# Kernel tuning notes

Hardware: AMD Instinct MI355X
Metric: run time of the kernel (lower is better)

The kernel has to match this reference:

```python
import jax, jax.numpy as jnp
import numpy as np

B, Q, K, D = 32, 1024, 1024, 64
MASK_VAL = -1000000.0  # matches torch source's -1e6 fill


def setup_inputs() -> dict:
    key = jax.random.key(0)
    kq, kk, kv, kl = jax.random.split(key, 4)
    return {
        "queries": jax.random.normal(kq, (B, Q, D), dtype=jnp.float32),
        "keys": jax.random.normal(kk, (B, K, D), dtype=jnp.float32),
        "values": jax.random.normal(kv, (B, K, D), dtype=jnp.float32),
        "valid_lens": jax.random.randint(kl, (B,), 1, K + 1, dtype=jnp.int64),
    }


def reference(queries, keys, values, valid_lens):
    d = queries.shape[-1]
    # [B, Q, K] scores
    scores = jnp.einsum("bqd,bkd->bqk", queries, keys) / jnp.sqrt(jnp.asarray(d, queries.dtype))
    # 1D valid_lens -> same length mask for every query row of a batch element
    kv_pos = jnp.arange(scores.shape[-1])  # [K]
    mask = kv_pos[None, None, :] < valid_lens[:, None, None]  # [B, 1, K] broadcast
    scores = jnp.where(mask, scores, MASK_VAL)
    attn = jax.nn.softmax(scores, axis=-1)
    # dropout p=0.0 -> identity
    return jnp.einsum("bqk,bkd->bqd", attn, values)
```

## Files before the change

### kernel.cpp

```cpp
#include <hip/hip_runtime.h>
#include <hip/hip_bf16.h>

#define NB 32
#define NQ 1024
#define NK 1024
#define ND 64
#define BK 64
#define M_FIX 16.0f

typedef __attribute__((ext_vector_type(8))) __bf16 bf16x8;
typedef __attribute__((ext_vector_type(8))) short  s16x8;
typedef __attribute__((ext_vector_type(4))) float  f32x4;

static __device__ __forceinline__ short f2bf(float f) {
  unsigned u = __builtin_bit_cast(unsigned, f);
  u += 0x7fffu + ((u >> 16) & 1u);
  return (short)(u >> 16);
}

static __device__ __forceinline__ int swzoff(int row, int gcol) {
  return row * 64 + (((gcol ^ (row & 7)) & 7) << 3);
}

#define GLD_LDS16(gp, lp)                                              \
  __builtin_amdgcn_global_load_lds(                                    \
      (const __attribute__((address_space(1))) void*)(gp),             \
      (__attribute__((address_space(3))) void*)(lp), 16, 0, 0)

__launch_bounds__(256)
__global__ void prep_kv(const float* __restrict__ Kp, const float* __restrict__ Vp,
                        const int* __restrict__ VLp,
                        short* __restrict__ Kb, short* __restrict__ Vt) {
  __shared__ __align__(16) short T[64 * 72];
  const int wg = blockIdx.x;
  const int b  = wg >> 4;
  const int kt = wg & 15;

  const bool is64 = (VLp[1] == 0);
  const int  len  = is64 ? VLp[2 * b] : VLp[b];
  if (kt * 64 >= len) return;

  const int tid = threadIdx.x;

  {
    const int key = tid >> 2, d0 = (tid & 3) * 16, g0 = (tid & 3) * 2;
    const float* src = Kp + ((size_t)(b * NK + kt * 64 + key)) * ND + d0;
    short out[16];
#pragma unroll
    for (int i = 0; i < 16; i += 4) {
      float4 v = *(const float4*)(src + i);
      out[i] = f2bf(v.x); out[i + 1] = f2bf(v.y);
      out[i + 2] = f2bf(v.z); out[i + 3] = f2bf(v.w);
    }
    short* dtile = Kb + ((size_t)(b * 16 + kt)) * 4096;
    *(s16x8*)&dtile[swzoff(key, g0)]     = *(const s16x8*)out;
    *(s16x8*)&dtile[swzoff(key, g0 + 1)] = *(const s16x8*)(out + 8);
  }

  {
    const int vkey = tid & 63, vd0 = (tid >> 6) * 16;
    const float* src = Vp + ((size_t)(b * NK + kt * 64 + vkey)) * ND + vd0;
#pragma unroll
    for (int i = 0; i < 4; ++i) {
      float4 v = *(const float4*)(src + i * 4);
      T[(vd0 + i * 4 + 0) * 72 + vkey] = f2bf(v.x);
      T[(vd0 + i * 4 + 1) * 72 + vkey] = f2bf(v.y);
      T[(vd0 + i * 4 + 2) * 72 + vkey] = f2bf(v.z);
      T[(vd0 + i * 4 + 3) * 72 + vkey] = f2bf(v.w);
    }
  }
  __syncthreads();
  {
    const int d = tid >> 2, c = (tid & 3) * 16, g0 = (tid & 3) * 2;
    short* vtile = Vt + ((size_t)(b * 16 + kt)) * 4096;
    *(s16x8*)&vtile[swzoff(d, g0)]     = *(const s16x8*)&T[d * 72 + c];
    *(s16x8*)&vtile[swzoff(d, g0 + 1)] = *(const s16x8*)&T[d * 72 + c + 8];
  }
}

__launch_bounds__(512, 4)
__global__ void attn_fwd(const float* __restrict__ Qp,
                         const short* __restrict__ Kb,
                         const short* __restrict__ Vt,
                         const int* __restrict__ VLp,
                         float* __restrict__ Op) {
  __shared__ __align__(16) short SM[40960];
  char* smb = (char*)SM;

  const int wg  = blockIdx.x;
  const int swz = (wg & 7) * 64 + (wg >> 3);
  const int b   = swz >> 4;
  const int qb  = swz & 15;

  const int tid  = threadIdx.x;
  const int wid  = tid >> 6;
  const int lane = tid & 63;
  const int l16  = lane & 15;
  const int grp  = lane >> 4;
  const int esw  = l16 & 7;
  const int qgrp = wid >> 1;
  const int par  = wid & 1;

  const bool is64 = (VLp[1] == 0);
  const int  len  = is64 ? VLp[2 * b] : VLp[b];
  const int  ntiles = (len + BK - 1) >> 6;
  const int  nsup   = (ntiles + 1) >> 1;
  const int  remLast = len - ((ntiles - 1) << 6);

  const float qscale = 0.125f * 1.44269504088896341f;

  bf16x8 qf[2];
  {
    const float* qsrc = Qp + ((size_t)(b * NQ + qb * 64 + qgrp * 16 + l16)) * ND + grp * 8;
#pragma unroll
    for (int k2 = 0; k2 < 2; ++k2) {
      float4 a = *(const float4*)(qsrc + k2 * 32);
      float4 c = *(const float4*)(qsrc + k2 * 32 + 4);
      s16x8 t;
      t[0] = f2bf(a.x * qscale); t[1] = f2bf(a.y * qscale);
      t[2] = f2bf(a.z * qscale); t[3] = f2bf(a.w * qscale);
      t[4] = f2bf(c.x * qscale); t[5] = f2bf(c.y * qscale);
      t[6] = f2bf(c.z * qscale); t[7] = f2bf(c.w * qscale);
      qf[k2] = __builtin_bit_cast(bf16x8, t);
    }
  }

  int ka0 = par * 8192 + l16 * 128 + ((((0 * 4 + grp) ^ esw)) << 4);
  int ka1 = par * 8192 + l16 * 128 + ((((1 * 4 + grp) ^ esw)) << 4);
  int pra[2], pwa[8];
#pragma unroll
  for (int ks = 0; ks < 2; ++ks)
    pra[ks] = 65536 + wid * 2048 + l16 * 128 + (((ks * 4 + grp) ^ esw) << 4);
#pragma unroll
  for (int n = 0; n < 4; ++n)
#pragma unroll
    for (int a = 0; a < 2; ++a)
      pwa[n * 2 + a] = 65536 + wid * 2048 + l16 * 128
                     + ((((2 * n + (grp >> 1)) ^ esw)) << 4) + (((2 * grp + a) & 3) << 2);

  const char* kgp = (const char*)(Kb + (size_t)b * 16 * 4096) + tid * 16;
  const char* vgp = (const char*)(Vt + (size_t)b * 16 * 4096) + tid * 16;
  const int dstW = wid * 1024;

  const f32x4 minit = {-M_FIX, -M_FIX, -M_FIX, -M_FIX};
  const f32x4 vzero = {0.f, 0.f, 0.f, 0.f};
  f32x4 oacc[4];
#pragma unroll
  for (int i = 0; i < 4; ++i) oacc[i] = vzero;
  float lrun = 0.f;

  int bufB = 0;

  GLD_LDS16(kgp,        smb + dstW);
  GLD_LDS16(kgp + 8192, smb + 8192 + dstW);
  GLD_LDS16(vgp,        smb + 32768 + dstW);
  GLD_LDS16(vgp + 8192, smb + 40960 + dstW);
  kgp += 16384; vgp += 16384;

  for (int it = 0; it < nsup; ++it) {
    asm volatile("s_waitcnt vmcnt(0)" ::: "memory");
    __builtin_amdgcn_sched_barrier(0);
    __builtin_amdgcn_s_barrier();
    __builtin_amdgcn_sched_barrier(0);

    if (it + 1 < nsup) {
      const int nb = bufB ^ 16384;
      GLD_LDS16(kgp,        smb + nb + dstW);
      GLD_LDS16(kgp + 8192, smb + nb + 8192 + dstW);
      GLD_LDS16(vgp,        smb + 32768 + nb + dstW);
      GLD_LDS16(vgp + 8192, smb + 32768 + nb + 8192 + dstW);
      kgp += 16384; vgp += 16384;
    }

    const int myt = 2 * it + par;
    if (myt < ntiles) {
      f32x4 sc[4];
      __builtin_amdgcn_s_setprio(1);
#pragma unroll
      for (int n = 0; n < 4; ++n) {
        bf16x8 kf0 = __builtin_bit_cast(bf16x8,
            *(const s16x8*)(smb + bufB + ka0 + n * 2048));
        bf16x8 kf1 = __builtin_bit_cast(bf16x8,
            *(const s16x8*)(smb + bufB + ka1 + n * 2048));
        f32x4 acc = __builtin_amdgcn_mfma_f32_16x16x32_bf16(kf0, qf[0], minit, 0, 0, 0);
        acc = __builtin_amdgcn_mfma_f32_16x16x32_bf16(kf1, qf[1], acc, 0, 0, 0);
        sc[n] = acc;
      }
      __builtin_amdgcn_s_setprio(0);

      if (myt == ntiles - 1) {
#pragma unroll
        for (int n = 0; n < 4; ++n)
#pragma unroll
          for (int r = 0; r < 4; ++r) {
            float x = (n * 16 + grp * 4 + r < remLast) ? sc[n][r] : -128.0f;
            float pv = exp2f(x);
            sc[n][r] = pv;
            lrun += pv;
          }
      } else {
#pragma unroll
        for (int n = 0; n < 4; ++n)
#pragma unroll
          for (int r = 0; r < 4; ++r) {
            float pv = exp2f(sc[n][r]);
            sc[n][r] = pv;
            lrun += pv;
          }
      }

#pragma unroll
      for (int n = 0; n < 4; ++n)
#pragma unroll
        for (int a = 0; a < 2; ++a) {
          int d;
          asm("v_cvt_pk_bf16_f32 %0, %1, %2"
              : "=v"(d) : "v"(sc[n][2 * a]), "v"(sc[n][2 * a + 1]));
          *(int*)(smb + pwa[n * 2 + a]) = d;
        }

      asm volatile("s_waitcnt lgkmcnt(0)" ::: "memory");
      __builtin_amdgcn_sched_barrier(0);

      bf16x8 pf[2];
#pragma unroll
      for (int ks = 0; ks < 2; ++ks)
        pf[ks] = __builtin_bit_cast(bf16x8, *(const s16x8*)(smb + pra[ks]));

      __builtin_amdgcn_s_setprio(1);
#pragma unroll
      for (int nd = 0; nd < 4; ++nd) {
        bf16x8 vf0 = __builtin_bit_cast(bf16x8,
            *(const s16x8*)(smb + bufB + ka0 + 32768 + nd * 2048));
        bf16x8 vf1 = __builtin_bit_cast(bf16x8,
            *(const s16x8*)(smb + bufB + ka1 + 32768 + nd * 2048));
        oacc[nd] = __builtin_amdgcn_mfma_f32_16x16x32_bf16(pf[0], vf0, oacc[nd], 0, 0, 0);
        oacc[nd] = __builtin_amdgcn_mfma_f32_16x16x32_bf16(pf[1], vf1, oacc[nd], 0, 0, 0);
      }
      __builtin_amdgcn_s_setprio(0);
    }

    bufB ^= 16384;
  }

  __syncthreads();
  float* CB = (float*)SM;
  const int crow = qgrp * 64 + lane;
  if (par == 1) {
    float* dst = CB + (size_t)crow * 20;
#pragma unroll
    for (int nd = 0; nd < 4; ++nd) *(f32x4*)(dst + nd * 4) = oacc[nd];
    dst[16] = lrun;
  }
  __syncthreads();
  if (par == 0) {
    const float* src = CB + (size_t)crow * 20;
#pragma unroll
    for (int nd = 0; nd < 4; ++nd) oacc[nd] += *(const f32x4*)(src + nd * 4);
    float l = lrun + src[16];
    l += __shfl_xor(l, 16);
    l += __shfl_xor(l, 32);
    const float inv = 1.0f / l;
    float invr[4];
#pragma unroll
    for (int r = 0; r < 4; ++r)
      invr[r] = __shfl(inv, (lane & 48) | (grp * 4 + r));

    float* obase = Op + ((size_t)(b * NQ + qb * 64 + qgrp * 16)) * ND;
#pragma unroll
    for (int nd = 0; nd < 4; ++nd)
#pragma unroll
      for (int r = 0; r < 4; ++r)
        obase[(grp * 4 + r) * ND + nd * 16 + l16] = oacc[nd][r] * invr[r];
  }
}

extern "C" void kernel_launch(void* const* d_in, const int* in_sizes, int n_in,
                              void* d_out, int out_size, void* d_ws, size_t ws_size,
                              hipStream_t stream) {
  const float* Qp = (const float*)d_in[0];
  const float* Kp = (const float*)d_in[1];
  const float* Vp = (const float*)d_in[2];
  const int*   VL = (const int*)d_in[3];
  float* Op = (float*)d_out;

  short* Kb = (short*)d_ws;
  short* Vt = Kb + (size_t)NB * NK * ND;

  prep_kv<<<dim3(NB * 16), dim3(256), 0, stream>>>(Kp, Vp, VL, Kb, Vt);
  attn_fwd<<<dim3(NB * 16), dim3(512), 0, stream>>>(Qp, Kb, Vt, VL, Op);
}
```

Baseline: 28.99 us.

## Split attention into 32-query blocks with 32-key tiles and 4-way KV split

Each workgroup now handles 32 query rows instead of 64, and the grid doubles to 1024 blocks. Each of 4 warps per query group processes its own 32-key tile, with K/V re-laid out into 32-key tiles in the prep kernel. Shared memory is halved and single-buffered with a second barrier before refilling, so launch bounds can allow 8 blocks per CU. The aim is more parallelism and occupancy for variable valid lengths. The cost is losing the double-buffered prefetch overlap, an extra barrier per iteration, and a 4-way partial-sum reduction at the end.

```diff
diff --git a/kernel.cpp b/kernel.cpp
--- a/kernel.cpp
+++ b/kernel.cpp
@@ -5,7 +5,6 @@
 #define NQ 1024
 #define NK 1024
 #define ND 64
-#define BK 64
 #define M_FIX 16.0f
 
 typedef __attribute__((ext_vector_type(8))) __bf16 bf16x8;
@@ -16,10 +15,6 @@
   unsigned u = __builtin_bit_cast(unsigned, f);
   u += 0x7fffu + ((u >> 16) & 1u);
   return (short)(u >> 16);
-}
-
-static __device__ __forceinline__ int swzoff(int row, int gcol) {
-  return row * 64 + (((gcol ^ (row & 7)) & 7) << 3);
 }
 
 #define GLD_LDS16(gp, lp)                                              \
@@ -44,6 +39,7 @@
 
   {
     const int key = tid >> 2, d0 = (tid & 3) * 16, g0 = (tid & 3) * 2;
+    const int row = key & 31, st = key >> 5;
     const float* src = Kp + ((size_t)(b * NK + kt * 64 + key)) * ND + d0;
     short out[16];
 #pragma unroll
@@ -52,9 +48,9 @@
       out[i] = f2bf(v.x); out[i + 1] = f2bf(v.y);
       out[i + 2] = f2bf(v.z); out[i + 3] = f2bf(v.w);
     }
-    short* dtile = Kb + ((size_t)(b * 16 + kt)) * 4096;
-    *(s16x8*)&dtile[swzoff(key, g0)]     = *(const s16x8*)out;
-    *(s16x8*)&dtile[swzoff(key, g0 + 1)] = *(const s16x8*)(out + 8);
+    short* dtile = Kb + ((size_t)(b * 32 + kt * 2 + st)) * 2048;
+    *(s16x8*)&dtile[row * 64 + (((g0    ) ^ (row & 7)) << 3)] = *(const s16x8*)out;
+    *(s16x8*)&dtile[row * 64 + (((g0 + 1) ^ (row & 7)) << 3)] = *(const s16x8*)(out + 8);
   }
 
   {
@@ -71,47 +67,50 @@
   }
   __syncthreads();
   {
-    const int d = tid >> 2, c = (tid & 3) * 16, g0 = (tid & 3) * 2;
-    short* vtile = Vt + ((size_t)(b * 16 + kt)) * 4096;
-    *(s16x8*)&vtile[swzoff(d, g0)]     = *(const s16x8*)&T[d * 72 + c];
-    *(s16x8*)&vtile[swzoff(d, g0 + 1)] = *(const s16x8*)&T[d * 72 + c + 8];
-  }
-}
-
-__launch_bounds__(512, 4)
+    const int d = tid >> 2, q4 = tid & 3;
+    const int st = q4 >> 1, g0 = (q4 & 1) * 2;
+    short* vtile = Vt + ((size_t)(b * 32 + kt * 2 + st)) * 2048;
+    const short* s = &T[d * 72 + q4 * 16];
+    *(s16x8*)&vtile[d * 32 + ((((g0    ) ^ (d & 3)) & 3) << 3)] = *(const s16x8*)s;
+    *(s16x8*)&vtile[d * 32 + ((((g0 + 1) ^ (d & 3)) & 3) << 3)] = *(const s16x8*)(s + 8);
+  }
+}
+
+__launch_bounds__(512, 8)
 __global__ void attn_fwd(const float* __restrict__ Qp,
                          const short* __restrict__ Kb,
                          const short* __restrict__ Vt,
                          const int* __restrict__ VLp,
                          float* __restrict__ Op) {
-  __shared__ __align__(16) short SM[40960];
+  __shared__ __align__(16) short SM[20480];
   char* smb = (char*)SM;
 
   const int wg  = blockIdx.x;
-  const int swz = (wg & 7) * 64 + (wg >> 3);
-  const int b   = swz >> 4;
-  const int qb  = swz & 15;
+  const int swz = (wg & 7) * 128 + (wg >> 3);
+  const int b   = swz >> 5;
+  const int qb  = swz & 31;
 
   const int tid  = threadIdx.x;
   const int wid  = tid >> 6;
   const int lane = tid & 63;
   const int l16  = lane & 15;
   const int grp  = lane >> 4;
-  const int esw  = l16 & 7;
-  const int qgrp = wid >> 1;
-  const int par  = wid & 1;
+  const int e7   = l16 & 7;
+  const int e3   = l16 & 3;
+  const int qgrp = wid >> 2;
+  const int par  = wid & 3;
 
   const bool is64 = (VLp[1] == 0);
   const int  len  = is64 ? VLp[2 * b] : VLp[b];
-  const int  ntiles = (len + BK - 1) >> 6;
-  const int  nsup   = (ntiles + 1) >> 1;
-  const int  remLast = len - ((ntiles - 1) << 6);
+  const int  ntiles = (len + 31) >> 5;
+  const int  nsup   = (ntiles + 3) >> 2;
+  const int  remLast = len - ((ntiles - 1) << 5);
 
   const float qscale = 0.125f * 1.44269504088896341f;
 
   bf16x8 qf[2];
   {
-    const float* qsrc = Qp + ((size_t)(b * NQ + qb * 64 + qgrp * 16 + l16)) * ND + grp * 8;
+    const float* qsrc = Qp + ((size_t)(b * NQ + qb * 32 + qgrp * 16 + l16)) * ND + grp * 8;
 #pragma unroll
     for (int k2 = 0; k2 < 2; ++k2) {
       float4 a = *(const float4*)(qsrc + k2 * 32);
@@ -125,21 +124,15 @@
     }
   }
 
-  int ka0 = par * 8192 + l16 * 128 + ((((0 * 4 + grp) ^ esw)) << 4);
-  int ka1 = par * 8192 + l16 * 128 + ((((1 * 4 + grp) ^ esw)) << 4);
-  int pra[2], pwa[8];
-#pragma unroll
-  for (int ks = 0; ks < 2; ++ks)
-    pra[ks] = 65536 + wid * 2048 + l16 * 128 + (((ks * 4 + grp) ^ esw) << 4);
-#pragma unroll
-  for (int n = 0; n < 4; ++n)
-#pragma unroll
-    for (int a = 0; a < 2; ++a)
-      pwa[n * 2 + a] = 65536 + wid * 2048 + l16 * 128
-                     + ((((2 * n + (grp >> 1)) ^ esw)) << 4) + (((2 * grp + a) & 3) << 2);
-
-  const char* kgp = (const char*)(Kb + (size_t)b * 16 * 4096) + tid * 16;
-  const char* vgp = (const char*)(Vt + (size_t)b * 16 * 4096) + tid * 16;
+  const int ka  = par * 4096 + l16 * 128;
+  const int kb0 = ka + (((0 + grp) ^ e7) << 4);
+  const int kb1 = ka + (((4 + grp) ^ e7) << 4);
+  const int va  = 16384 + par * 4096 + l16 * 64 + (((grp ^ e3) & 3) << 4);
+  const int pb  = 32768 + wid * 1024 + l16 * 64;
+  const int pra = pb + (((grp ^ e3) & 3) << 4);
+
+  const char* kgp = (const char*)(Kb + (size_t)b * 32 * 2048) + tid * 16;
+  const char* vgp = (const char*)(Vt + (size_t)b * 32 * 2048) + tid * 16;
   const int dstW = wid * 1024;
 
   const f32x4 minit = {-M_FIX, -M_FIX, -M_FIX, -M_FIX};
@@ -149,12 +142,10 @@
   for (int i = 0; i < 4; ++i) oacc[i] = vzero;
   float lrun = 0.f;
 
-  int bufB = 0;
-
   GLD_LDS16(kgp,        smb + dstW);
   GLD_LDS16(kgp + 8192, smb + 8192 + dstW);
-  GLD_LDS16(vgp,        smb + 32768 + dstW);
-  GLD_LDS16(vgp + 8192, smb + 40960 + dstW);
+  GLD_LDS16(vgp,        smb + 16384 + dstW);
+  GLD_LDS16(vgp + 8192, smb + 24576 + dstW);
   kgp += 16384; vgp += 16384;
 
   for (int it = 0; it < nsup; ++it) {
@@ -163,25 +154,14 @@
     __builtin_amdgcn_s_barrier();
     __builtin_amdgcn_sched_barrier(0);
 
-    if (it + 1 < nsup) {
-      const int nb = bufB ^ 16384;
-      GLD_LDS16(kgp,        smb + nb + dstW);
-      GLD_LDS16(kgp + 8192, smb + nb + 8192 + dstW);
-      GLD_LDS16(vgp,        smb + 32768 + nb + dstW);
-      GLD_LDS16(vgp + 8192, smb + 32768 + nb + 8192 + dstW);
-      kgp += 16384; vgp += 16384;
-    }
-
-    const int myt = 2 * it + par;
+    const int myt = 4 * it + par;
     if (myt < ntiles) {
-      f32x4 sc[4];
+      f32x4 sc[2];
       __builtin_amdgcn_s_setprio(1);
 #pragma unroll
-      for (int n = 0; n < 4; ++n) {
-        bf16x8 kf0 = __builtin_bit_cast(bf16x8,
-            *(const s16x8*)(smb + bufB + ka0 + n * 2048));
-        bf16x8 kf1 = __builtin_bit_cast(bf16x8,
-            *(const s16x8*)(smb + bufB + ka1 + n * 2048));
+      for (int n = 0; n < 2; ++n) {
+        bf16x8 kf0 = __builtin_bit_cast(bf16x8, *(const s16x8*)(smb + kb0 + n * 2048));
+        bf16x8 kf1 = __builtin_bit_cast(bf16x8, *(const s16x8*)(smb + kb1 + n * 2048));
         f32x4 acc = __builtin_amdgcn_mfma_f32_16x16x32_bf16(kf0, qf[0], minit, 0, 0, 0);
         acc = __builtin_amdgcn_mfma_f32_16x16x32_bf16(kf1, qf[1], acc, 0, 0, 0);
         sc[n] = acc;
@@ -190,7 +170,7 @@
 
       if (myt == ntiles - 1) {
 #pragma unroll
-        for (int n = 0; n < 4; ++n)
+        for (int n = 0; n < 2; ++n)
 #pragma unroll
           for (int r = 0; r < 4; ++r) {
             float x = (n * 16 + grp * 4 + r < remLast) ? sc[n][r] : -128.0f;
@@ -200,7 +180,7 @@
           }
       } else {
 #pragma unroll
-        for (int n = 0; n < 4; ++n)
+        for (int n = 0; n < 2; ++n)
 #pragma unroll
           for (int r = 0; r < 4; ++r) {
             float pv = exp2f(sc[n][r]);
@@ -210,54 +190,62 @@
       }
 
 #pragma unroll
-      for (int n = 0; n < 4; ++n)
+      for (int n = 0; n < 2; ++n)
 #pragma unroll
         for (int a = 0; a < 2; ++a) {
           int d;
           asm("v_cvt_pk_bf16_f32 %0, %1, %2"
               : "=v"(d) : "v"(sc[n][2 * a]), "v"(sc[n][2 * a + 1]));
-          *(int*)(smb + pwa[n * 2 + a]) = d;
+          *(int*)(smb + pb + ((((2 * n + (grp >> 1)) ^ e3) & 3) << 4)
+                        + (((grp * 2 + a) & 3) << 2)) = d;
         }
 
       asm volatile("s_waitcnt lgkmcnt(0)" ::: "memory");
       __builtin_amdgcn_sched_barrier(0);
 
-      bf16x8 pf[2];
-#pragma unroll
-      for (int ks = 0; ks < 2; ++ks)
-        pf[ks] = __builtin_bit_cast(bf16x8, *(const s16x8*)(smb + pra[ks]));
+      bf16x8 pf = __builtin_bit_cast(bf16x8, *(const s16x8*)(smb + pra));
 
       __builtin_amdgcn_s_setprio(1);
 #pragma unroll
       for (int nd = 0; nd < 4; ++nd) {
-        bf16x8 vf0 = __builtin_bit_cast(bf16x8,
-            *(const s16x8*)(smb + bufB + ka0 + 32768 + nd * 2048));
-        bf16x8 vf1 = __builtin_bit_cast(bf16x8,
-            *(const s16x8*)(smb + bufB + ka1 + 32768 + nd * 2048));
-        oacc[nd] = __builtin_amdgcn_mfma_f32_16x16x32_bf16(pf[0], vf0, oacc[nd], 0, 0, 0);
-        oacc[nd] = __builtin_amdgcn_mfma_f32_16x16x32_bf16(pf[1], vf1, oacc[nd], 0, 0, 0);
+        bf16x8 vf = __builtin_bit_cast(bf16x8, *(const s16x8*)(smb + va + nd * 1024));
+        oacc[nd] = __builtin_amdgcn_mfma_f32_16x16x32_bf16(pf, vf, oacc[nd], 0, 0, 0);
       }
       __builtin_amdgcn_s_setprio(0);
     }
 
-    bufB ^= 16384;
+    asm volatile("s_waitcnt lgkmcnt(0)" ::: "memory");
+    __builtin_amdgcn_sched_barrier(0);
+    __builtin_amdgcn_s_barrier();
+    __builtin_amdgcn_sched_barrier(0);
+
+    if (it + 1 < nsup) {
+      GLD_LDS16(kgp,        smb + dstW);
+      GLD_LDS16(kgp + 8192, smb + 8192 + dstW);
+      GLD_LDS16(vgp,        smb + 16384 + dstW);
+      GLD_LDS16(vgp + 8192, smb + 24576 + dstW);
+      kgp += 16384; vgp += 16384;
+    }
   }
 
   __syncthreads();
   float* CB = (float*)SM;
-  const int crow = qgrp * 64 + lane;
-  if (par == 1) {
-    float* dst = CB + (size_t)crow * 20;
+  if (par != 0) {
+    float* dst = CB + (size_t)(((par - 1) * 2 + qgrp) * 64 + lane) * 20;
 #pragma unroll
     for (int nd = 0; nd < 4; ++nd) *(f32x4*)(dst + nd * 4) = oacc[nd];
     dst[16] = lrun;
   }
   __syncthreads();
   if (par == 0) {
-    const float* src = CB + (size_t)crow * 20;
-#pragma unroll
-    for (int nd = 0; nd < 4; ++nd) oacc[nd] += *(const f32x4*)(src + nd * 4);
-    float l = lrun + src[16];
+    float l = lrun;
+#pragma unroll
+    for (int w = 0; w < 3; ++w) {
+      const float* src = CB + (size_t)((w * 2 + qgrp) * 64 + lane) * 20;
+#pragma unroll
+      for (int nd = 0; nd < 4; ++nd) oacc[nd] += *(const f32x4*)(src + nd * 4);
+      l += src[16];
+    }
     l += __shfl_xor(l, 16);
     l += __shfl_xor(l, 32);
     const float inv = 1.0f / l;
@@ -266,7 +254,7 @@
     for (int r = 0; r < 4; ++r)
       invr[r] = __shfl(inv, (lane & 48) | (grp * 4 + r));
 
-    float* obase = Op + ((size_t)(b * NQ + qb * 64 + qgrp * 16)) * ND;
+    float* obase = Op + ((size_t)(b * NQ + qb * 32 + qgrp * 16)) * ND;
 #pragma unroll
     for (int nd = 0; nd < 4; ++nd)
 #pragma unroll
@@ -288,5 +276,5 @@
   short* Vt = Kb + (size_t)NB * NK * ND;
 
   prep_kv<<<dim3(NB * 16), dim3(256), 0, stream>>>(Kp, Vp, VL, Kb, Vt);
-  attn_fwd<<<dim3(NB * 16), dim3(512), 0, stream>>>(Qp, Kb, Vt, VL, Op);
-}
+  attn_fwd<<<dim3(NB * 32), dim3(512), 0, stream>>>(Qp, Kb, Vt, VL, Op);
+}
```

After: 35.52 us. 1.23x slower.

## Keep P in registers and compute PV as transposed 16x16x16 MFMA

Applied to the files above, without the earlier changes.

Removes the LDS round trip for the softmax probabilities: P is packed to bf16 in registers and fed directly as the B operand of 16x16x16 MFMAs computing O^T, with V read in a new 4-element swizzled layout written by prep_kv. This also drops the P scratch region from shared memory, lowering LDS use, and lets the epilogue write float4 rows without shuffling the normalizer. The cost is twice as many MFMA instructions of a lower-throughput shape, smaller 8-byte LDS reads for V, and an added s_nop pad before the final barrier.

```diff
diff --git a/kernel.cpp b/kernel.cpp
--- a/kernel.cpp
+++ b/kernel.cpp
@@ -10,7 +10,9 @@
 
 typedef __attribute__((ext_vector_type(8))) __bf16 bf16x8;
 typedef __attribute__((ext_vector_type(8))) short  s16x8;
+typedef __attribute__((ext_vector_type(4))) short  s16x4;
 typedef __attribute__((ext_vector_type(4))) float  f32x4;
+typedef __attribute__((ext_vector_type(2))) int    i32x2;
 
 static __device__ __forceinline__ short f2bf(float f) {
   unsigned u = __builtin_bit_cast(unsigned, f);
@@ -26,6 +28,10 @@
   __builtin_amdgcn_global_load_lds(                                    \
       (const __attribute__((address_space(1))) void*)(gp),             \
       (__attribute__((address_space(3))) void*)(lp), 16, 0, 0)
+
+#define MFMA16(acc, va_, vb_)                                          \
+  asm("v_mfma_f32_16x16x16_bf16 %0, %1, %2, %0"                        \
+      : "+v"(acc) : "v"(va_), "v"(vb_))
 
 __launch_bounds__(256)
 __global__ void prep_kv(const float* __restrict__ Kp, const float* __restrict__ Vp,
@@ -71,10 +77,13 @@
   }
   __syncthreads();
   {
-    const int d = tid >> 2, c = (tid & 3) * 16, g0 = (tid & 3) * 2;
+    const int d = tid >> 2, q4 = tid & 3;
     short* vtile = Vt + ((size_t)(b * 16 + kt)) * 4096;
-    *(s16x8*)&vtile[swzoff(d, g0)]     = *(const s16x8*)&T[d * 72 + c];
-    *(s16x8*)&vtile[swzoff(d, g0 + 1)] = *(const s16x8*)&T[d * 72 + c + 8];
+    const short* s = &T[d * 72 + q4 * 16];
+#pragma unroll
+    for (int i = 0; i < 4; ++i)
+      *(s16x4*)&vtile[d * 64 + (((4 * q4 + i) ^ (d & 15)) << 2)] =
+          *(const s16x4*)(s + 4 * i);
   }
 }
 
@@ -84,7 +93,7 @@
                          const short* __restrict__ Vt,
                          const int* __restrict__ VLp,
                          float* __restrict__ Op) {
-  __shared__ __align__(16) short SM[40960];
+  __shared__ __align__(16) short SM[32768];
   char* smb = (char*)SM;
 
   const int wg  = blockIdx.x;
@@ -125,18 +134,12 @@
     }
   }
 
-  int ka0 = par * 8192 + l16 * 128 + ((((0 * 4 + grp) ^ esw)) << 4);
-  int ka1 = par * 8192 + l16 * 128 + ((((1 * 4 + grp) ^ esw)) << 4);
-  int pra[2], pwa[8];
-#pragma unroll
-  for (int ks = 0; ks < 2; ++ks)
-    pra[ks] = 65536 + wid * 2048 + l16 * 128 + (((ks * 4 + grp) ^ esw) << 4);
+  const int ka0 = par * 8192 + l16 * 128 + (((0 + grp) ^ esw) << 4);
+  const int ka1 = par * 8192 + l16 * 128 + (((4 + grp) ^ esw) << 4);
+  int van[4];
 #pragma unroll
   for (int n = 0; n < 4; ++n)
-#pragma unroll
-    for (int a = 0; a < 2; ++a)
-      pwa[n * 2 + a] = 65536 + wid * 2048 + l16 * 128
-                     + ((((2 * n + (grp >> 1)) ^ esw)) << 4) + (((2 * grp + a) & 3) << 2);
+    van[n] = 32768 + par * 8192 + l16 * 128 + (((4 * n + grp) ^ l16) << 3);
 
   const char* kgp = (const char*)(Kb + (size_t)b * 16 * 4096) + tid * 16;
   const char* vgp = (const char*)(Vt + (size_t)b * 16 * 4096) + tid * 16;
@@ -188,9 +191,10 @@
       }
       __builtin_amdgcn_s_setprio(0);
 
+      i32x2 pk[4];
       if (myt == ntiles - 1) {
 #pragma unroll
-        for (int n = 0; n < 4; ++n)
+        for (int n = 0; n < 4; ++n) {
 #pragma unroll
           for (int r = 0; r < 4; ++r) {
             float x = (n * 16 + grp * 4 + r < remLast) ? sc[n][r] : -128.0f;
@@ -198,50 +202,48 @@
             sc[n][r] = pv;
             lrun += pv;
           }
+          int plo, phi;
+          asm("v_cvt_pk_bf16_f32 %0, %1, %2" : "=v"(plo) : "v"(sc[n][0]), "v"(sc[n][1]));
+          asm("v_cvt_pk_bf16_f32 %0, %1, %2" : "=v"(phi) : "v"(sc[n][2]), "v"(sc[n][3]));
+          pk[n][0] = plo; pk[n][1] = phi;
+        }
       } else {
 #pragma unroll
-        for (int n = 0; n < 4; ++n)
+        for (int n = 0; n < 4; ++n) {
 #pragma unroll
           for (int r = 0; r < 4; ++r) {
             float pv = exp2f(sc[n][r]);
             sc[n][r] = pv;
             lrun += pv;
           }
+          int plo, phi;
+          asm("v_cvt_pk_bf16_f32 %0, %1, %2" : "=v"(plo) : "v"(sc[n][0]), "v"(sc[n][1]));
+          asm("v_cvt_pk_bf16_f32 %0, %1, %2" : "=v"(phi) : "v"(sc[n][2]), "v"(sc[n][3]));
+          pk[n][0] = plo; pk[n][1] = phi;
+        }
       }
-
-#pragma unroll
-      for (int n = 0; n < 4; ++n)
-#pragma unroll
-        for (int a = 0; a < 2; ++a) {
-          int d;
-          asm("v_cvt_pk_bf16_f32 %0, %1, %2"
-              : "=v"(d) : "v"(sc[n][2 * a]), "v"(sc[n][2 * a + 1]));
-          *(int*)(smb + pwa[n * 2 + a]) = d;
-        }
-
-      asm volatile("s_waitcnt lgkmcnt(0)" ::: "memory");
       __builtin_amdgcn_sched_barrier(0);
 
-      bf16x8 pf[2];
-#pragma unroll
-      for (int ks = 0; ks < 2; ++ks)
-        pf[ks] = __builtin_bit_cast(bf16x8, *(const s16x8*)(smb + pra[ks]));
-
       __builtin_amdgcn_s_setprio(1);
 #pragma unroll
-      for (int nd = 0; nd < 4; ++nd) {
-        bf16x8 vf0 = __builtin_bit_cast(bf16x8,
-            *(const s16x8*)(smb + bufB + ka0 + 32768 + nd * 2048));
-        bf16x8 vf1 = __builtin_bit_cast(bf16x8,
-            *(const s16x8*)(smb + bufB + ka1 + 32768 + nd * 2048));
-        oacc[nd] = __builtin_amdgcn_mfma_f32_16x16x32_bf16(pf[0], vf0, oacc[nd], 0, 0, 0);
-        oacc[nd] = __builtin_amdgcn_mfma_f32_16x16x32_bf16(pf[1], vf1, oacc[nd], 0, 0, 0);
+      for (int m = 0; m < 4; ++m) {
+        i32x2 vf0 = *(const i32x2*)(smb + bufB + van[0] + m * 2048);
+        i32x2 vf1 = *(const i32x2*)(smb + bufB + van[1] + m * 2048);
+        i32x2 vf2 = *(const i32x2*)(smb + bufB + van[2] + m * 2048);
+        i32x2 vf3 = *(const i32x2*)(smb + bufB + van[3] + m * 2048);
+        MFMA16(oacc[m], vf0, pk[0]);
+        MFMA16(oacc[m], vf1, pk[1]);
+        MFMA16(oacc[m], vf2, pk[2]);
+        MFMA16(oacc[m], vf3, pk[3]);
       }
       __builtin_amdgcn_s_setprio(0);
     }
 
     bufB ^= 16384;
   }
+
+  __builtin_amdgcn_sched_barrier(0);
+  asm volatile("s_nop 7\n\ts_nop 7" ::: "memory");
 
   __syncthreads();
   float* CB = (float*)SM;
@@ -249,29 +251,26 @@
   if (par == 1) {
     float* dst = CB + (size_t)crow * 20;
 #pragma unroll
-    for (int nd = 0; nd < 4; ++nd) *(f32x4*)(dst + nd * 4) = oacc[nd];
+    for (int m = 0; m < 4; ++m) *(f32x4*)(dst + m * 4) = oacc[m];
     dst[16] = lrun;
   }
   __syncthreads();
   if (par == 0) {
     const float* src = CB + (size_t)crow * 20;
 #pragma unroll
-    for (int nd = 0; nd < 4; ++nd) oacc[nd] += *(const f32x4*)(src + nd * 4);
+    for (int m = 0; m < 4; ++m) oacc[m] += *(const f32x4*)(src + m * 4);
     float l = lrun + src[16];
     l += __shfl_xor(l, 16);
     l += __shfl_xor(l, 32);
     const float inv = 1.0f / l;
-    float invr[4];
-#pragma unroll
-    for (int r = 0; r < 4; ++r)
-      invr[r] = __shfl(inv, (lane & 48) | (grp * 4 + r));
-
-    float* obase = Op + ((size_t)(b * NQ + qb * 64 + qgrp * 16)) * ND;
-#pragma unroll
-    for (int nd = 0; nd < 4; ++nd)
-#pragma unroll
-      for (int r = 0; r < 4; ++r)
-        obase[(grp * 4 + r) * ND + nd * 16 + l16] = oacc[nd][r] * invr[r];
+
+    float* obase = Op + ((size_t)(b * NQ + qb * 64 + qgrp * 16 + l16)) * ND;
+#pragma unroll
+    for (int m = 0; m < 4; ++m) {
+      float4 o = {oacc[m][0] * inv, oacc[m][1] * inv,
+                  oacc[m][2] * inv, oacc[m][3] * inv};
+      *(float4*)(obase + m * 16 + grp * 4) = o;
+    }
   }
 }
 
```

Measured after the change: 29.57 us. +2.0%, slower.
